# Optimization experiments

Hardware: AMD Instinct MI355X
Metric: run time of the kernel (lower is better)

The kernel has to match this reference:

```python
import jax, jax.numpy as jnp
import numpy as np

DIM = 512
HEADS = 8
HEAD_DIM = DIM // HEADS  # 64
NUM_ENC = 32             # num_encoding_channels
ENC_RANGE = 1.0
OFFSETS = (0, 512, 2560) # B=2 point clouds, num_points=(512, 2048)
B = len(OFFSETS) - 1
M = 2048                 # max num_points -> padded length
TOTAL = OFFSETS[-1]      # 2560 total points
ENC_IN = NUM_ENC * 3 + 3 # 99 (concat_input=True)


def setup_inputs() -> dict:
    key = jax.random.key(0)
    ks = jax.random.split(key, 6)
    return {
        "features": jax.random.normal(ks[0], (TOTAL, DIM), jnp.float32),
        "coordinates": jax.random.uniform(ks[1], (TOTAL, 3), jnp.float32),
        "qkv_w": jax.random.normal(ks[2], (3 * DIM, DIM), jnp.float32) * (DIM ** -0.5),
        "proj_w": jax.random.normal(ks[3], (DIM, DIM), jnp.float32) * (DIM ** -0.5),
        "proj_b": jnp.zeros((DIM,), jnp.float32),
        "pos_w": jax.random.normal(ks[4], (HEAD_DIM, ENC_IN), jnp.float32) * (ENC_IN ** -0.5),
        "pos_b": jnp.zeros((HEAD_DIM,), jnp.float32),
        "offsets": jnp.array(OFFSETS, jnp.int32),
    }


def reference(features, coordinates, qkv_w, proj_w, proj_b, pos_w, pos_b, offsets):
    # ragged -> padded index math (replaces cat_to_pad / pad_to_cat Python loops)
    pt = jnp.arange(TOTAL)
    b_idx = jnp.searchsorted(offsets, pt, side='right') - 1   # batch id per point
    w_idx = pt - offsets[b_idx]                                # within-batch position
    num_points = offsets[1:] - offsets[:-1]                    # [B]

    # SinusoidalEncoding(num_channels=32, concat_input=True) + Linear -> head_dim
    half = NUM_ENC // 2
    freqs = (2.0 ** jnp.arange(half, dtype=jnp.float32)) * jnp.pi / ENC_RANGE
    sc = coordinates[..., None] * freqs                        # [T, 3, half]
    enc = jnp.concatenate([jnp.sin(sc), jnp.cos(sc)], -1).reshape(TOTAL, 3 * NUM_ENC)
    enc = jnp.concatenate([enc, coordinates], -1)              # [T, 99]
    pos = enc @ pos_w.T + pos_b                                # [T, head_dim]

    feat_pad = jnp.zeros((B, M, DIM), features.dtype).at[b_idx, w_idx].set(features)
    pos_pad = jnp.zeros((B, M, HEAD_DIM), pos.dtype).at[b_idx, w_idx].set(pos)

    # offset_to_mask: mask[b, :, :offsets[b], :offsets[b]] = -inf (cumulative offsets!)
    r = jnp.arange(M)
    off_b = offsets[:-1]                                       # [B]
    blocked = (r[None, :, None] < off_b[:, None, None]) & (r[None, None, :] < off_b[:, None, None])
    mask = jnp.where(blocked, -jnp.inf, 0.0)[:, None]          # [B, 1, M, M]

    # attention
    qkv = (feat_pad @ qkv_w.T).reshape(B, M, 3, HEADS, HEAD_DIM)
    qkv = jnp.transpose(qkv, (2, 0, 3, 1, 4))                  # [3, B, H, M, hd]
    q, k, v = qkv[0], qkv[1], qkv[2]
    q = q + pos_pad[:, None]                                   # broadcast over heads
    k = k + pos_pad[:, None]
    scale = HEAD_DIM ** -0.5
    scores = jnp.einsum('bhqd,bhkd->bhqk', q, k) * scale + mask
    attn = jax.nn.softmax(scores, axis=-1)
    y = jnp.einsum('bhqk,bhkd->bhqd', attn, v)                 # [B, H, M, hd]
    y = jnp.transpose(y, (0, 2, 1, 3)).reshape(B, M, DIM)
    y = y @ proj_w.T + proj_b

    # zero_out_points: x[b, num_points[b]:] = 0
    valid = r[None, :] < num_points[:, None]
    y = jnp.where(valid[..., None], y, 0.0)

    # pad_to_cat back to ragged [total_N, C]
    return y[b_idx, w_idx]
```

## Files before the change

kernel.cpp:

```cpp
#include <hip/hip_runtime.h>
#include <math.h>

#define TOTAL 2560
#define NEG_BIG (-1e30f)
#define LOG2E_8 0.18033688011112042f

typedef __bf16 bf16x8 __attribute__((ext_vector_type(8)));
typedef float f32x4 __attribute__((ext_vector_type(4)));
typedef unsigned short ushort8v __attribute__((ext_vector_type(8)));
typedef unsigned short ushort4v __attribute__((ext_vector_type(4)));

__device__ inline unsigned short f2bf(float f) {
    unsigned u = __builtin_bit_cast(unsigned, f);
    u += 0x7fff + ((u >> 16) & 1);
    return (unsigned short)(u >> 16);
}

__device__ inline void gload16(const void* g, void* l) {
    __builtin_amdgcn_global_load_lds(
        (const __attribute__((address_space(1))) void*)g,
        (__attribute__((address_space(3))) void*)l, 16, 0, 0);
}

__global__ __launch_bounds__(256) void pos_cast_kernel(
    const float* __restrict__ coords,
    const float* __restrict__ pos_w,
    const float* __restrict__ pos_b,
    const float* __restrict__ f,  const float* __restrict__ qw, const float* __restrict__ pw,
    float* __restrict__ pos_out,
    unsigned short* __restrict__ fb, unsigned short* __restrict__ qwb, unsigned short* __restrict__ pwb)
{
    const int bx = blockIdx.x;
    if (bx < 640) {
        __shared__ float enc[4][100];
        const int wv   = threadIdx.x >> 6;
        const int lane = threadIdx.x & 63;
        const int p = bx * 4 + wv;
        const float c0 = coords[p * 3 + 0];
        const float c1 = coords[p * 3 + 1];
        const float c2 = coords[p * 3 + 2];
        for (int i = lane; i < 99; i += 64) {
            float v;
            if (i < 96) {
                const int d = i >> 5;
                const int j = i & 31;
                const float cv = (d == 0) ? c0 : ((d == 1) ? c1 : c2);
                const float freq = exp2f((float)(j & 15)) * 3.14159265358979323846f;
                const float sc = cv * freq;
                v = (j < 16) ? sinf(sc) : cosf(sc);
            } else {
                v = (i == 96) ? c0 : ((i == 97) ? c1 : c2);
            }
            enc[wv][i] = v;
        }
        float acc = pos_b[lane];
        const float* w = pos_w + lane * 99;
        for (int i = 0; i < 99; ++i) acc = fmaf(enc[wv][i], w[i], acc);
        pos_out[p * 64 + lane] = acc;
    } else {
        const int s = (bx - 640) * 256 + threadIdx.x;
        const float* src; unsigned short* dst; int ls;
        if (s < 163840)      { src = f;  dst = fb;  ls = s; }
        else if (s < 262144) { src = qw; dst = qwb; ls = s - 163840; }
        else                 { src = pw; dst = pwb; ls = s - 262144; }
        const float4 x0 = *(const float4*)(src + ls * 8);
        const float4 x1 = *(const float4*)(src + ls * 8 + 4);
        ushort8v o;
        o[0] = f2bf(x0.x); o[1] = f2bf(x0.y); o[2] = f2bf(x0.z); o[3] = f2bf(x0.w);
        o[4] = f2bf(x1.x); o[5] = f2bf(x1.y); o[6] = f2bf(x1.z); o[7] = f2bf(x1.w);
        *(ushort8v*)(dst + ls * 8) = o;
    }
}

__global__ __launch_bounds__(256) void qkv_mfma_kernel(
    const unsigned short* __restrict__ A,
    const unsigned short* __restrict__ Bm,
    const float* __restrict__ pos,
    unsigned short* __restrict__ q_ws,
    unsigned short* __restrict__ k_ws,
    unsigned short* __restrict__ vt_ws)
{
    __shared__ unsigned short Abuf[2][64 * 64];
    __shared__ unsigned short Bbuf[2][64 * 64];
    const int m0 = blockIdx.x * 64;
    const int n0 = blockIdx.y * 64;
    const int t = threadIdx.x;
    const int w = t >> 6, lane = t & 63;
    const int wr = w >> 1, wc = w & 1;
    const int c = lane & 15, g = lane >> 4;

    auto STAGE = [&](int kt, int cur) {
#pragma unroll
        for (int i = 0; i < 2; ++i) {
            const int off = w * 2048 + i * 1024;
            const int ba  = off + lane * 16;
            const int row = ba >> 7;
            const int slot = (ba & 127) >> 4;
            gload16(A  + (m0 + row) * 512 + kt * 64 + ((slot ^ (row & 7)) * 8),
                    (char*)&Abuf[cur][0] + off);
            gload16(Bm + (n0 + row) * 512 + kt * 64 + ((slot ^ (row & 7)) * 8),
                    (char*)&Bbuf[cur][0] + off);
        }
    };

    f32x4 acc[2][2];
#pragma unroll
    for (int mi = 0; mi < 2; ++mi)
#pragma unroll
        for (int ni = 0; ni < 2; ++ni) acc[mi][ni] = (f32x4){0.f, 0.f, 0.f, 0.f};

    STAGE(0, 0);
    int cur = 0;
    for (int kt = 0; kt < 8; ++kt) {
        __syncthreads();
        if (kt + 1 < 8) STAGE(kt + 1, cur ^ 1);
#pragma unroll
        for (int kk = 0; kk < 2; ++kk) {
            bf16x8 af[2], bfr[2];
#pragma unroll
            for (int mi = 0; mi < 2; ++mi) {
                const int row = wr * 32 + mi * 16 + c;
                af[mi] = *(const bf16x8*)&Abuf[cur][row * 64 + ((g + 4 * kk) ^ (row & 7)) * 8];
            }
#pragma unroll
            for (int ni = 0; ni < 2; ++ni) {
                const int row = wc * 32 + ni * 16 + c;
                bfr[ni] = *(const bf16x8*)&Bbuf[cur][row * 64 + ((g + 4 * kk) ^ (row & 7)) * 8];
            }
#pragma unroll
            for (int mi = 0; mi < 2; ++mi)
#pragma unroll
                for (int ni = 0; ni < 2; ++ni)
                    acc[mi][ni] = __builtin_amdgcn_mfma_f32_16x16x32_bf16(af[mi], bfr[ni], acc[mi][ni], 0, 0, 0);
        }
        cur ^= 1;
    }

    const int which = n0 >> 9;
    const int h = (n0 >> 6) & 7;
#pragma unroll
    for (int mi = 0; mi < 2; ++mi)
#pragma unroll
        for (int ni = 0; ni < 2; ++ni) {
            const int dd = wc * 32 + ni * 16 + c;
            const int p0 = m0 + wr * 32 + mi * 16 + 4 * g;
            if (which == 2) {
                ushort4v o4;
#pragma unroll
                for (int r = 0; r < 4; ++r) o4[r] = f2bf(acc[mi][ni][r]);
                *(ushort4v*)(vt_ws + (h * 64 + dd) * TOTAL + p0) = o4;
            } else {
#pragma unroll
                for (int r = 0; r < 4; ++r) {
                    const int p = p0 + r;
                    const float v = acc[mi][ni][r] + pos[p * 64 + dd];
                    const int idx = (h * TOTAL + p) * 64 + dd;
                    if (which == 0) q_ws[idx] = f2bf(v);
                    else            k_ws[idx] = f2bf(v);
                }
            }
        }
}

__global__ __launch_bounds__(256) void attn_kernel(
    const unsigned short* __restrict__ q_ws,
    const unsigned short* __restrict__ k_ws,
    const unsigned short* __restrict__ vt_ws,
    unsigned short* __restrict__ y)
{
    const int bx = blockIdx.x;
    const int h  = bx & 7;
    const int qt = bx >> 3;

    const int t    = threadIdx.x;
    const int w    = t >> 6;
    const int lane = t & 63;
    const int g    = lane >> 4;
    const int c    = lane & 15;
    const int c7   = c & 7;

    __shared__ unsigned short Kbuf[256 * 64];
    __shared__ unsigned short Vbuf[2][64 * 256];
    __shared__ unsigned short P_lds[64][264];

    const int nphase = (qt < 8) ? 2 : 1;
    int cur = 0;

    for (int phase = 0; phase < nphase; ++phase) {
        const int base = phase ? 0 : 512;
        const int nkt  = phase ? 2 : 8;
        const int kt0  = (!phase && qt < 8) ? 2 : 0;
        const float extra = phase ? 1536.0f : 0.0f;

        const unsigned short* Kg = k_ws + (h * TOTAL + base) * 64;
        const unsigned short* Vg = vt_ws + h * 64 * TOTAL + base;

        const unsigned short* Qrow = q_ws + ((h * TOTAL) + base + qt * 64 + 16 * w + c) * 64;
        const bf16x8 qa0 = *(const bf16x8*)(Qrow + 8 * g);
        const bf16x8 qa1 = *(const bf16x8*)(Qrow + 8 * g + 32);

        float m_old = NEG_BIG, l_old = 0.f;
        f32x4 o_acc[4];
#pragma unroll
        for (int n = 0; n < 4; ++n) o_acc[n] = (f32x4){0.f, 0.f, 0.f, 0.f};

        auto STAGE_K = [&](int kt) {
#pragma unroll
            for (int i = 0; i < 8; ++i) {
                const int off = w * 8192 + i * 1024;
                const int ba  = off + lane * 16;
                const int row = ba >> 7;
                const int slot = (ba & 127) >> 4;
                gload16(Kg + (kt * 256 + row) * 64 + ((slot ^ (row & 7)) * 8),
                        (char*)&Kbuf[0] + off);
            }
        };
        auto STAGE_V = [&](int kt, int vb) {
#pragma unroll
            for (int i = 0; i < 8; ++i) {
                const int off = w * 8192 + i * 1024;
                const int ba  = off + lane * 16;
                const int dd  = ba >> 9;
                const int slot = (ba & 511) >> 4;
                gload16(Vg + dd * TOTAL + kt * 256 + ((slot ^ (dd & 7)) * 8),
                        (char*)&Vbuf[vb][0] + off);
            }
        };

        if (phase) __syncthreads();
        STAGE_K(kt0);
        STAGE_V(kt0, cur);

        for (int kt = kt0; kt < nkt; ++kt) {
            __syncthreads();

            f32x4 s_acc[16];
#pragma unroll
            for (int n = 0; n < 16; ++n) {
                const int row = 16 * n + c;
                const bf16x8 kb0 = *(const bf16x8*)&Kbuf[row * 64 + ((g + 0) ^ c7) * 8];
                const bf16x8 kb1 = *(const bf16x8*)&Kbuf[row * 64 + ((g + 4) ^ c7) * 8];
                f32x4 a = __builtin_amdgcn_mfma_f32_16x16x32_bf16(kb0, qa0, (f32x4){0.f,0.f,0.f,0.f}, 0, 0, 0);
                s_acc[n] = __builtin_amdgcn_mfma_f32_16x16x32_bf16(kb1, qa1, a, 0, 0, 0);
            }
            __syncthreads();
            if (kt + 1 < nkt) STAGE_K(kt + 1);

            f32x4 m4 = s_acc[0];
#pragma unroll
            for (int n = 1; n < 16; ++n)
#pragma unroll
                for (int r = 0; r < 4; ++r) m4[r] = fmaxf(m4[r], s_acc[n][r]);
            float tm = fmaxf(fmaxf(m4[0], m4[1]), fmaxf(m4[2], m4[3])) * LOG2E_8;
            tm = fmaxf(tm, __shfl_xor(tm, 16));
            tm = fmaxf(tm, __shfl_xor(tm, 32));
            if (!__all(tm <= m_old + 8.0f)) {
                const float m_new = fmaxf(m_old, tm);
                const float corr = exp2f(m_old - m_new);
                float corr_r[4];
#pragma unroll
                for (int r = 0; r < 4; ++r) corr_r[r] = __shfl(corr, 4 * g + r);
#pragma unroll
                for (int n = 0; n < 4; ++n)
#pragma unroll
                    for (int r = 0; r < 4; ++r) o_acc[n][r] *= corr_r[r];
                l_old *= corr;
                m_old = m_new;
            }
            float rs = 0.f;
#pragma unroll
            for (int n = 0; n < 16; ++n)
#pragma unroll
                for (int r = 0; r < 4; ++r) {
                    const float pv = exp2f(fmaf(s_acc[n][r], LOG2E_8, -m_old));
                    s_acc[n][r] = pv;
                    rs += pv;
                }
            rs += __shfl_xor(rs, 16);
            rs += __shfl_xor(rs, 32);
            l_old += rs;

#pragma unroll
            for (int n = 0; n < 16; ++n) {
                ushort4v pk;
#pragma unroll
                for (int r = 0; r < 4; ++r) pk[r] = f2bf(s_acc[n][r]);
                *(ushort4v*)&P_lds[16 * w + c][16 * n + 4 * g] = pk;
            }

            if (kt + 1 < nkt) STAGE_V(kt + 1, cur ^ 1);

#pragma unroll
            for (int kk = 0; kk < 8; ++kk) {
                const bf16x8 pa = *(const bf16x8*)&P_lds[16 * w + c][8 * g + 32 * kk];
                const int vslot = (g + 4 * kk) ^ c7;
#pragma unroll
                for (int n = 0; n < 4; ++n) {
                    const bf16x8 vb = *(const bf16x8*)&Vbuf[cur][(16 * n + c) * 256 + vslot * 8];
                    o_acc[n] = __builtin_amdgcn_mfma_f32_16x16x32_bf16(pa, vb, o_acc[n], 0, 0, 0);
                }
            }
            cur ^= 1;
        }

        float inv_own;
        if (extra > 0.f) {
            const float mn  = fmaxf(m_old, 0.f);
            const float ccf = exp2f(m_old - mn);
            const float l   = l_old * ccf + extra * exp2f(-mn);
            inv_own = ccf / l;
        } else {
            inv_own = 1.0f / l_old;
        }
        float inv_r[4];
#pragma unroll
        for (int r = 0; r < 4; ++r) inv_r[r] = __shfl(inv_own, 4 * g + r);
        unsigned short* yb = y + (base + qt * 64 + 16 * w) * 512 + h * 64;
#pragma unroll
        for (int n = 0; n < 4; ++n)
#pragma unroll
            for (int r = 0; r < 4; ++r)
                yb[(4 * g + r) * 512 + 16 * n + c] = f2bf(o_acc[n][r] * inv_r[r]);
    }
}

__global__ __launch_bounds__(256) void proj_mfma_kernel(
    const unsigned short* __restrict__ A,
    const unsigned short* __restrict__ Bm,
    const float* __restrict__ bias,
    float* __restrict__ out)
{
    __shared__ unsigned short Abuf[2][64 * 64];
    __shared__ unsigned short Bbuf[2][64 * 64];
    const int m0 = blockIdx.x * 64;
    const int n0 = blockIdx.y * 64;
    const int t = threadIdx.x;
    const int w = t >> 6, lane = t & 63;
    const int wr = w >> 1, wc = w & 1;
    const int c = lane & 15, g = lane >> 4;

    auto STAGE = [&](int kt, int cur) {
#pragma unroll
        for (int i = 0; i < 2; ++i) {
            const int off = w * 2048 + i * 1024;
            const int ba  = off + lane * 16;
            const int row = ba >> 7;
            const int slot = (ba & 127) >> 4;
            gload16(A  + (m0 + row) * 512 + kt * 64 + ((slot ^ (row & 7)) * 8),
                    (char*)&Abuf[cur][0] + off);
            gload16(Bm + (n0 + row) * 512 + kt * 64 + ((slot ^ (row & 7)) * 8),
                    (char*)&Bbuf[cur][0] + off);
        }
    };

    f32x4 acc[2][2];
#pragma unroll
    for (int mi = 0; mi < 2; ++mi)
#pragma unroll
        for (int ni = 0; ni < 2; ++ni) acc[mi][ni] = (f32x4){0.f, 0.f, 0.f, 0.f};

    STAGE(0, 0);
    int cur = 0;
    for (int kt = 0; kt < 8; ++kt) {
        __syncthreads();
        if (kt + 1 < 8) STAGE(kt + 1, cur ^ 1);
#pragma unroll
        for (int kk = 0; kk < 2; ++kk) {
            bf16x8 af[2], bfr[2];
#pragma unroll
            for (int mi = 0; mi < 2; ++mi) {
                const int row = wr * 32 + mi * 16 + c;
                af[mi] = *(const bf16x8*)&Abuf[cur][row * 64 + ((g + 4 * kk) ^ (row & 7)) * 8];
            }
#pragma unroll
            for (int ni = 0; ni < 2; ++ni) {
                const int row = wc * 32 + ni * 16 + c;
                bfr[ni] = *(const bf16x8*)&Bbuf[cur][row * 64 + ((g + 4 * kk) ^ (row & 7)) * 8];
            }
#pragma unroll
            for (int mi = 0; mi < 2; ++mi)
#pragma unroll
                for (int ni = 0; ni < 2; ++ni)
                    acc[mi][ni] = __builtin_amdgcn_mfma_f32_16x16x32_bf16(af[mi], bfr[ni], acc[mi][ni], 0, 0, 0);
        }
        cur ^= 1;
    }

#pragma unroll
    for (int mi = 0; mi < 2; ++mi)
#pragma unroll
        for (int ni = 0; ni < 2; ++ni) {
            const int col = n0 + wc * 32 + ni * 16 + c;
            const float bv = bias[col];
#pragma unroll
            for (int r = 0; r < 4; ++r) {
                const int p = m0 + wr * 32 + mi * 16 + 4 * g + r;
                out[p * 512 + col] = acc[mi][ni][r] + bv;
            }
        }
}

extern "C" void kernel_launch(void* const* d_in, const int* in_sizes, int n_in,
                              void* d_out, int out_size, void* d_ws, size_t ws_size,
                              hipStream_t stream) {
    const float* features = (const float*)d_in[0];
    const float* coords   = (const float*)d_in[1];
    const float* qkv_w    = (const float*)d_in[2];
    const float* proj_w   = (const float*)d_in[3];
    const float* proj_b   = (const float*)d_in[4];
    const float* pos_w    = (const float*)d_in[5];
    const float* pos_b    = (const float*)d_in[6];
    float* out = (float*)d_out;

    float* pos_ws = (float*)d_ws;
    unsigned short* feat_bf  = (unsigned short*)(pos_ws + TOTAL * 64);
    unsigned short* qkvw_bf  = feat_bf + 2560 * 512;
    unsigned short* projw_bf = qkvw_bf + 1536 * 512;
    unsigned short* q_ws  = projw_bf + 512 * 512;
    unsigned short* k_ws  = q_ws  + 8 * TOTAL * 64;
    unsigned short* vt_ws = k_ws  + 8 * TOTAL * 64;
    unsigned short* y_bf  = vt_ws + 8 * TOTAL * 64;

    pos_cast_kernel<<<dim3(1792), dim3(256), 0, stream>>>(
        coords, pos_w, pos_b, features, qkv_w, proj_w,
        pos_ws, feat_bf, qkvw_bf, projw_bf);
    qkv_mfma_kernel<<<dim3(40, 24), dim3(256), 0, stream>>>(
        feat_bf, qkvw_bf, pos_ws, q_ws, k_ws, vt_ws);
    attn_kernel<<<dim3(256), dim3(256), 0, stream>>>(q_ws, k_ws, vt_ws, y_bf);
    proj_mfma_kernel<<<dim3(40, 8), dim3(256), 0, stream>>>(
        y_bf, projw_bf, proj_b, out);
}
```

Before: 64.41 us.

## Split attention over key range with partial softmax and combine kernel

The attention kernel now processes 128 query rows per block, two 16-row groups per wave, so each staged K/V tile is reused for twice as many queries. For the 2048-point cloud the key range is split into two halves across blocks, writing unnormalized fp32 partial outputs and (max, sum) statistics. A new combine kernel merges the halves and converts to bf16. The aim is better load balance and K/V reuse at the same grid size. The cost is an extra kernel launch and fp32 partial-output traffic through global memory.

```diff
diff --git a/kernel.cpp b/kernel.cpp
--- a/kernel.cpp
+++ b/kernel.cpp
@@ -162,15 +162,17 @@
         }
 }
 
-__global__ __launch_bounds__(256) void attn_kernel(
+__global__ __launch_bounds__(256) void attn_part_kernel(
     const unsigned short* __restrict__ q_ws,
     const unsigned short* __restrict__ k_ws,
     const unsigned short* __restrict__ vt_ws,
-    unsigned short* __restrict__ y)
+    float* __restrict__ o_part,
+    float2* __restrict__ ml2)
 {
-    const int bx = blockIdx.x;
-    const int h  = bx & 7;
-    const int qt = bx >> 3;
+    const int bx  = blockIdx.x;
+    const int h   = bx & 7;
+    const int qt2 = (bx >> 3) & 15;
+    const int sp  = bx >> 7;
 
     const int t    = threadIdx.x;
     const int w    = t >> 6;
@@ -183,26 +185,36 @@
     __shared__ unsigned short Vbuf[2][64 * 256];
     __shared__ unsigned short P_lds[64][264];
 
-    const int nphase = (qt < 8) ? 2 : 1;
+    const int nphase = (sp == 0 && qt2 < 4) ? 2 : 1;
     int cur = 0;
 
     for (int phase = 0; phase < nphase; ++phase) {
         const int base = phase ? 0 : 512;
-        const int nkt  = phase ? 2 : 8;
-        const int kt0  = (!phase && qt < 8) ? 2 : 0;
+        int t0, t1;
+        if (phase) { t0 = 0; t1 = 2; }
+        else {
+            const int kt0 = (qt2 < 4) ? 2 : 0;
+            t0 = sp ? 4 : kt0;
+            t1 = sp ? 8 : 4;
+        }
         const float extra = phase ? 1536.0f : 0.0f;
 
         const unsigned short* Kg = k_ws + (h * TOTAL + base) * 64;
         const unsigned short* Vg = vt_ws + h * 64 * TOTAL + base;
 
-        const unsigned short* Qrow = q_ws + ((h * TOTAL) + base + qt * 64 + 16 * w + c) * 64;
-        const bf16x8 qa0 = *(const bf16x8*)(Qrow + 8 * g);
-        const bf16x8 qa1 = *(const bf16x8*)(Qrow + 8 * g + 32);
-
-        float m_old = NEG_BIG, l_old = 0.f;
-        f32x4 o_acc[4];
-#pragma unroll
-        for (int n = 0; n < 4; ++n) o_acc[n] = (f32x4){0.f, 0.f, 0.f, 0.f};
+        const unsigned short* Qrow = q_ws + ((h * TOTAL) + base + qt2 * 128 + 32 * w + c) * 64;
+        const bf16x8 qlo0 = *(const bf16x8*)(Qrow + 8 * g);
+        const bf16x8 qlo1 = *(const bf16x8*)(Qrow + 8 * g + 32);
+        const bf16x8 qhi0 = *(const bf16x8*)(Qrow + 16 * 64 + 8 * g);
+        const bf16x8 qhi1 = *(const bf16x8*)(Qrow + 16 * 64 + 8 * g + 32);
+
+        float m_lo = NEG_BIG, l_lo = 0.f, m_hi = NEG_BIG, l_hi = 0.f;
+        f32x4 o_lo[4], o_hi[4];
+#pragma unroll
+        for (int n = 0; n < 4; ++n) {
+            o_lo[n] = (f32x4){0.f, 0.f, 0.f, 0.f};
+            o_hi[n] = (f32x4){0.f, 0.f, 0.f, 0.f};
+        }
 
         auto STAGE_K = [&](int kt) {
 #pragma unroll
@@ -227,30 +239,22 @@
             }
         };
 
-        if (phase) __syncthreads();
-        STAGE_K(kt0);
-        STAGE_V(kt0, cur);
-
-        for (int kt = kt0; kt < nkt; ++kt) {
-            __syncthreads();
-
-            f32x4 s_acc[16];
+        auto QK = [&](f32x4* s, const bf16x8& qa0, const bf16x8& qa1) {
 #pragma unroll
             for (int n = 0; n < 16; ++n) {
                 const int row = 16 * n + c;
                 const bf16x8 kb0 = *(const bf16x8*)&Kbuf[row * 64 + ((g + 0) ^ c7) * 8];
                 const bf16x8 kb1 = *(const bf16x8*)&Kbuf[row * 64 + ((g + 4) ^ c7) * 8];
                 f32x4 a = __builtin_amdgcn_mfma_f32_16x16x32_bf16(kb0, qa0, (f32x4){0.f,0.f,0.f,0.f}, 0, 0, 0);
-                s_acc[n] = __builtin_amdgcn_mfma_f32_16x16x32_bf16(kb1, qa1, a, 0, 0, 0);
-            }
-            __syncthreads();
-            if (kt + 1 < nkt) STAGE_K(kt + 1);
-
-            f32x4 m4 = s_acc[0];
+                s[n] = __builtin_amdgcn_mfma_f32_16x16x32_bf16(kb1, qa1, a, 0, 0, 0);
+            }
+        };
+        auto SOFTMAX = [&](f32x4* s, float& m_old, float& l_old, f32x4* o) {
+            f32x4 m4 = s[0];
 #pragma unroll
             for (int n = 1; n < 16; ++n)
 #pragma unroll
-                for (int r = 0; r < 4; ++r) m4[r] = fmaxf(m4[r], s_acc[n][r]);
+                for (int r = 0; r < 4; ++r) m4[r] = fmaxf(m4[r], s[n][r]);
             float tm = fmaxf(fmaxf(m4[0], m4[1]), fmaxf(m4[2], m4[3])) * LOG2E_8;
             tm = fmaxf(tm, __shfl_xor(tm, 16));
             tm = fmaxf(tm, __shfl_xor(tm, 32));
@@ -263,7 +267,7 @@
 #pragma unroll
                 for (int n = 0; n < 4; ++n)
 #pragma unroll
-                    for (int r = 0; r < 4; ++r) o_acc[n][r] *= corr_r[r];
+                    for (int r = 0; r < 4; ++r) o[n][r] *= corr_r[r];
                 l_old *= corr;
                 m_old = m_new;
             }
@@ -272,56 +276,132 @@
             for (int n = 0; n < 16; ++n)
 #pragma unroll
                 for (int r = 0; r < 4; ++r) {
-                    const float pv = exp2f(fmaf(s_acc[n][r], LOG2E_8, -m_old));
-                    s_acc[n][r] = pv;
+                    const float pv = exp2f(fmaf(s[n][r], LOG2E_8, -m_old));
+                    s[n][r] = pv;
                     rs += pv;
                 }
             rs += __shfl_xor(rs, 16);
             rs += __shfl_xor(rs, 32);
             l_old += rs;
-
+        };
+        auto PWRITE = [&](const f32x4* s) {
 #pragma unroll
             for (int n = 0; n < 16; ++n) {
                 ushort4v pk;
 #pragma unroll
-                for (int r = 0; r < 4; ++r) pk[r] = f2bf(s_acc[n][r]);
+                for (int r = 0; r < 4; ++r) pk[r] = f2bf(s[n][r]);
                 *(ushort4v*)&P_lds[16 * w + c][16 * n + 4 * g] = pk;
             }
-
-            if (kt + 1 < nkt) STAGE_V(kt + 1, cur ^ 1);
-
+        };
+        auto PV = [&](f32x4* o, int vb) {
 #pragma unroll
             for (int kk = 0; kk < 8; ++kk) {
                 const bf16x8 pa = *(const bf16x8*)&P_lds[16 * w + c][8 * g + 32 * kk];
                 const int vslot = (g + 4 * kk) ^ c7;
 #pragma unroll
                 for (int n = 0; n < 4; ++n) {
-                    const bf16x8 vb = *(const bf16x8*)&Vbuf[cur][(16 * n + c) * 256 + vslot * 8];
-                    o_acc[n] = __builtin_amdgcn_mfma_f32_16x16x32_bf16(pa, vb, o_acc[n], 0, 0, 0);
+                    const bf16x8 vv = *(const bf16x8*)&Vbuf[vb][(16 * n + c) * 256 + vslot * 8];
+                    o[n] = __builtin_amdgcn_mfma_f32_16x16x32_bf16(pa, vv, o[n], 0, 0, 0);
                 }
             }
+        };
+
+        if (phase) __syncthreads();
+        STAGE_K(t0);
+        STAGE_V(t0, cur);
+
+        for (int kt = t0; kt < t1; ++kt) {
+            __syncthreads();
+            f32x4 s_acc[16];
+            QK(s_acc, qlo0, qlo1);
+            SOFTMAX(s_acc, m_lo, l_lo, o_lo);
+            PWRITE(s_acc);
+            QK(s_acc, qhi0, qhi1);
+            __syncthreads();
+            if (kt + 1 < t1) STAGE_K(kt + 1);
+            PV(o_lo, cur);
+            SOFTMAX(s_acc, m_hi, l_hi, o_hi);
+            PWRITE(s_acc);
+            if (kt + 1 < t1) STAGE_V(kt + 1, cur ^ 1);
+            PV(o_hi, cur);
             cur ^= 1;
         }
 
-        float inv_own;
-        if (extra > 0.f) {
-            const float mn  = fmaxf(m_old, 0.f);
-            const float ccf = exp2f(m_old - mn);
-            const float l   = l_old * ccf + extra * exp2f(-mn);
-            inv_own = ccf / l;
+        if (phase) {
+            const float mn_l = fmaxf(m_lo, 0.f);
+            const float cl   = exp2f(m_lo - mn_l);
+            const float il   = cl / (l_lo * cl + extra * exp2f(-mn_l));
+            const float mn_h = fmaxf(m_hi, 0.f);
+            const float ch   = exp2f(m_hi - mn_h);
+            const float ih   = ch / (l_hi * ch + extra * exp2f(-mn_h));
+            float ilr[4], ihr[4];
+#pragma unroll
+            for (int r = 0; r < 4; ++r) {
+                ilr[r] = __shfl(il, 4 * g + r);
+                ihr[r] = __shfl(ih, 4 * g + r);
+            }
+            float* op = o_part + (size_t)(qt2 * 128 + 32 * w) * 512 + h * 64;
+#pragma unroll
+            for (int n = 0; n < 4; ++n)
+#pragma unroll
+                for (int r = 0; r < 4; ++r) {
+                    op[(4 * g + r) * 512 + 16 * n + c]      = o_lo[n][r] * ilr[r];
+                    op[(16 + 4 * g + r) * 512 + 16 * n + c] = o_hi[n][r] * ihr[r];
+                }
         } else {
-            inv_own = 1.0f / l_old;
-        }
-        float inv_r[4];
-#pragma unroll
-        for (int r = 0; r < 4; ++r) inv_r[r] = __shfl(inv_own, 4 * g + r);
-        unsigned short* yb = y + (base + qt * 64 + 16 * w) * 512 + h * 64;
-#pragma unroll
-        for (int n = 0; n < 4; ++n)
-#pragma unroll
-            for (int r = 0; r < 4; ++r)
-                yb[(4 * g + r) * 512 + 16 * n + c] = f2bf(o_acc[n][r] * inv_r[r]);
+            float* op = o_part + (size_t)sp * (TOTAL * 512)
+                      + (size_t)(512 + qt2 * 128 + 32 * w) * 512 + h * 64;
+#pragma unroll
+            for (int n = 0; n < 4; ++n)
+#pragma unroll
+                for (int r = 0; r < 4; ++r) {
+                    op[(4 * g + r) * 512 + 16 * n + c]      = o_lo[n][r];
+                    op[(16 + 4 * g + r) * 512 + 16 * n + c] = o_hi[n][r];
+                }
+            if (lane < 16) {
+                const int p = 512 + qt2 * 128 + 32 * w + c;
+                ml2[((size_t)sp * TOTAL + p) * 8 + h]      = make_float2(m_lo, l_lo);
+                ml2[((size_t)sp * TOTAL + p + 16) * 8 + h] = make_float2(m_hi, l_hi);
+            }
+        }
     }
+}
+
+__global__ __launch_bounds__(256) void combine_kernel(
+    const float* __restrict__ o_part,
+    const float2* __restrict__ ml2,
+    unsigned short* __restrict__ y)
+{
+    const int e = blockIdx.x * 256 + threadIdx.x;
+    const int p = e >> 6;
+    const int seg = e & 63;
+    const size_t bo = (size_t)p * 512 + seg * 8;
+    const float4 a0 = *(const float4*)(o_part + bo);
+    const float4 a1 = *(const float4*)(o_part + bo + 4);
+    ushort8v y8;
+    if (p < 512) {
+        y8[0] = f2bf(a0.x); y8[1] = f2bf(a0.y); y8[2] = f2bf(a0.z); y8[3] = f2bf(a0.w);
+        y8[4] = f2bf(a1.x); y8[5] = f2bf(a1.y); y8[6] = f2bf(a1.z); y8[7] = f2bf(a1.w);
+    } else {
+        const int h = seg >> 3;
+        const float2 v0 = ml2[(size_t)p * 8 + h];
+        const float2 v1 = ml2[(size_t)(TOTAL + p) * 8 + h];
+        const float mt = fmaxf(v0.x, v1.x);
+        const float c0 = exp2f(v0.x - mt), c1 = exp2f(v1.x - mt);
+        const float inv = 1.0f / fmaf(v0.y, c0, v1.y * c1);
+        const float f0 = c0 * inv, f1 = c1 * inv;
+        const float4 b0 = *(const float4*)(o_part + (size_t)TOTAL * 512 + bo);
+        const float4 b1 = *(const float4*)(o_part + (size_t)TOTAL * 512 + bo + 4);
+        y8[0] = f2bf(fmaf(a0.x, f0, b0.x * f1));
+        y8[1] = f2bf(fmaf(a0.y, f0, b0.y * f1));
+        y8[2] = f2bf(fmaf(a0.z, f0, b0.z * f1));
+        y8[3] = f2bf(fmaf(a0.w, f0, b0.w * f1));
+        y8[4] = f2bf(fmaf(a1.x, f0, b1.x * f1));
+        y8[5] = f2bf(fmaf(a1.y, f0, b1.y * f1));
+        y8[6] = f2bf(fmaf(a1.z, f0, b1.z * f1));
+        y8[7] = f2bf(fmaf(a1.w, f0, b1.w * f1));
+    }
+    *(ushort8v*)(y + bo) = y8;
 }
 
 __global__ __launch_bounds__(256) void proj_mfma_kernel(
@@ -419,14 +499,18 @@
     unsigned short* q_ws  = projw_bf + 512 * 512;
     unsigned short* k_ws  = q_ws  + 8 * TOTAL * 64;
     unsigned short* vt_ws = k_ws  + 8 * TOTAL * 64;
-    unsigned short* y_bf  = vt_ws + 8 * TOTAL * 64;
+    float* o_part = (float*)(vt_ws + 8 * TOTAL * 64);
+    float2* ml2   = (float2*)(o_part + 2 * TOTAL * 512);
+    unsigned short* y_bf = (unsigned short*)(ml2 + 2 * TOTAL * 8);
 
     pos_cast_kernel<<<dim3(1792), dim3(256), 0, stream>>>(
         coords, pos_w, pos_b, features, qkv_w, proj_w,
         pos_ws, feat_bf, qkvw_bf, projw_bf);
     qkv_mfma_kernel<<<dim3(40, 24), dim3(256), 0, stream>>>(
         feat_bf, qkvw_bf, pos_ws, q_ws, k_ws, vt_ws);
-    attn_kernel<<<dim3(256), dim3(256), 0, stream>>>(q_ws, k_ws, vt_ws, y_bf);
+    attn_part_kernel<<<dim3(256), dim3(256), 0, stream>>>(
+        q_ws, k_ws, vt_ws, o_part, ml2);
+    combine_kernel<<<dim3(640), dim3(256), 0, stream>>>(o_part, ml2, y_bf);
     proj_mfma_kernel<<<dim3(40, 8), dim3(256), 0, stream>>>(
         y_bf, projw_bf, proj_b, out);
 }
```

Measured after the change: 78.59 us. +22.0%, slower.

## Split attention key tile across two wave groups with LDS softmax merge

Applied to the files above, without the earlier changes.

Doubles the attention block to 512 threads. Each group of four waves processes half of every 256-key tile, and the two partial online-softmax states (max, sum, output) are merged through shared memory at the end. This aims to raise wave-level parallelism and latency hiding per CU, since the grid has only 256 blocks. In exchange it adds shared memory (Om, Oml), a merge pass and a barrier. Each wave tracks its own running max, so the rescaling logic is duplicated.

```diff
diff --git a/kernel.cpp b/kernel.cpp
--- a/kernel.cpp
+++ b/kernel.cpp
@@ -162,7 +162,7 @@
         }
 }
 
-__global__ __launch_bounds__(256) void attn_kernel(
+__global__ __launch_bounds__(512) void attn_kernel(
     const unsigned short* __restrict__ q_ws,
     const unsigned short* __restrict__ k_ws,
     const unsigned short* __restrict__ vt_ws,
@@ -174,6 +174,9 @@
 
     const int t    = threadIdx.x;
     const int w    = t >> 6;
+    const int wp   = w & 3;
+    const int half = w >> 2;
+    const int koff = half * 128;
     const int lane = t & 63;
     const int g    = lane >> 4;
     const int c    = lane & 15;
@@ -182,6 +185,8 @@
     __shared__ unsigned short Kbuf[256 * 64];
     __shared__ unsigned short Vbuf[2][64 * 256];
     __shared__ unsigned short P_lds[64][264];
+    __shared__ float  Om[64 * 64];
+    __shared__ float2 Oml[64];
 
     const int nphase = (qt < 8) ? 2 : 1;
     int cur = 0;
@@ -195,7 +200,7 @@
         const unsigned short* Kg = k_ws + (h * TOTAL + base) * 64;
         const unsigned short* Vg = vt_ws + h * 64 * TOTAL + base;
 
-        const unsigned short* Qrow = q_ws + ((h * TOTAL) + base + qt * 64 + 16 * w + c) * 64;
+        const unsigned short* Qrow = q_ws + ((h * TOTAL) + base + qt * 64 + 16 * wp + c) * 64;
         const bf16x8 qa0 = *(const bf16x8*)(Qrow + 8 * g);
         const bf16x8 qa1 = *(const bf16x8*)(Qrow + 8 * g + 32);
 
@@ -206,8 +211,8 @@
 
         auto STAGE_K = [&](int kt) {
 #pragma unroll
-            for (int i = 0; i < 8; ++i) {
-                const int off = w * 8192 + i * 1024;
+            for (int i = 0; i < 4; ++i) {
+                const int off = w * 4096 + i * 1024;
                 const int ba  = off + lane * 16;
                 const int row = ba >> 7;
                 const int slot = (ba & 127) >> 4;
@@ -217,8 +222,8 @@
         };
         auto STAGE_V = [&](int kt, int vb) {
 #pragma unroll
-            for (int i = 0; i < 8; ++i) {
-                const int off = w * 8192 + i * 1024;
+            for (int i = 0; i < 4; ++i) {
+                const int off = w * 4096 + i * 1024;
                 const int ba  = off + lane * 16;
                 const int dd  = ba >> 9;
                 const int slot = (ba & 511) >> 4;
@@ -234,10 +239,10 @@
         for (int kt = kt0; kt < nkt; ++kt) {
             __syncthreads();
 
-            f32x4 s_acc[16];
-#pragma unroll
-            for (int n = 0; n < 16; ++n) {
-                const int row = 16 * n + c;
+            f32x4 s_acc[8];
+#pragma unroll
+            for (int n = 0; n < 8; ++n) {
+                const int row = koff + 16 * n + c;
                 const bf16x8 kb0 = *(const bf16x8*)&Kbuf[row * 64 + ((g + 0) ^ c7) * 8];
                 const bf16x8 kb1 = *(const bf16x8*)&Kbuf[row * 64 + ((g + 4) ^ c7) * 8];
                 f32x4 a = __builtin_amdgcn_mfma_f32_16x16x32_bf16(kb0, qa0, (f32x4){0.f,0.f,0.f,0.f}, 0, 0, 0);
@@ -248,7 +253,7 @@
 
             f32x4 m4 = s_acc[0];
 #pragma unroll
-            for (int n = 1; n < 16; ++n)
+            for (int n = 1; n < 8; ++n)
 #pragma unroll
                 for (int r = 0; r < 4; ++r) m4[r] = fmaxf(m4[r], s_acc[n][r]);
             float tm = fmaxf(fmaxf(m4[0], m4[1]), fmaxf(m4[2], m4[3])) * LOG2E_8;
@@ -269,7 +274,7 @@
             }
             float rs = 0.f;
 #pragma unroll
-            for (int n = 0; n < 16; ++n)
+            for (int n = 0; n < 8; ++n)
 #pragma unroll
                 for (int r = 0; r < 4; ++r) {
                     const float pv = exp2f(fmaf(s_acc[n][r], LOG2E_8, -m_old));
@@ -281,46 +286,69 @@
             l_old += rs;
 
 #pragma unroll
-            for (int n = 0; n < 16; ++n) {
+            for (int n = 0; n < 8; ++n) {
                 ushort4v pk;
 #pragma unroll
                 for (int r = 0; r < 4; ++r) pk[r] = f2bf(s_acc[n][r]);
-                *(ushort4v*)&P_lds[16 * w + c][16 * n + 4 * g] = pk;
+                *(ushort4v*)&P_lds[16 * wp + c][koff + 16 * n + 4 * g] = pk;
             }
 
             if (kt + 1 < nkt) STAGE_V(kt + 1, cur ^ 1);
 
 #pragma unroll
-            for (int kk = 0; kk < 8; ++kk) {
-                const bf16x8 pa = *(const bf16x8*)&P_lds[16 * w + c][8 * g + 32 * kk];
-                const int vslot = (g + 4 * kk) ^ c7;
+            for (int kk = 0; kk < 4; ++kk) {
+                const bf16x8 pa = *(const bf16x8*)&P_lds[16 * wp + c][koff + 8 * g + 32 * kk];
+                const int vgrp = ((koff >> 3) + 4 * kk + g) ^ c7;
 #pragma unroll
                 for (int n = 0; n < 4; ++n) {
-                    const bf16x8 vb = *(const bf16x8*)&Vbuf[cur][(16 * n + c) * 256 + vslot * 8];
+                    const bf16x8 vb = *(const bf16x8*)&Vbuf[cur][(16 * n + c) * 256 + vgrp * 8];
                     o_acc[n] = __builtin_amdgcn_mfma_f32_16x16x32_bf16(pa, vb, o_acc[n], 0, 0, 0);
                 }
             }
             cur ^= 1;
         }
 
-        float inv_own;
-        if (extra > 0.f) {
-            const float mn  = fmaxf(m_old, 0.f);
-            const float ccf = exp2f(m_old - mn);
-            const float l   = l_old * ccf + extra * exp2f(-mn);
-            inv_own = ccf / l;
-        } else {
-            inv_own = 1.0f / l_old;
-        }
-        float inv_r[4];
-#pragma unroll
-        for (int r = 0; r < 4; ++r) inv_r[r] = __shfl(inv_own, 4 * g + r);
-        unsigned short* yb = y + (base + qt * 64 + 16 * w) * 512 + h * 64;
-#pragma unroll
-        for (int n = 0; n < 4; ++n)
-#pragma unroll
-            for (int r = 0; r < 4; ++r)
-                yb[(4 * g + r) * 512 + 16 * n + c] = f2bf(o_acc[n][r] * inv_r[r]);
+        if (half == 1) {
+            const int pr = wp * 16;
+#pragma unroll
+            for (int n = 0; n < 4; ++n)
+#pragma unroll
+                for (int r = 0; r < 4; ++r)
+                    Om[(pr + 4 * g + r) * 64 + 16 * n + c] = o_acc[n][r];
+            if (g == 0) Oml[pr + c] = make_float2(m_old, l_old);
+        }
+        __syncthreads();
+        if (half == 0) {
+            const int pr = wp * 16;
+            const float2 o2 = Oml[pr + c];
+            const float mm = fmaxf(m_old, o2.x);
+            const float f0 = exp2f(m_old - mm), f1 = exp2f(o2.x - mm);
+            float l = l_old * f0 + o2.y * f1;
+            float so = 1.f;
+            if (extra > 0.f) {
+                const float mn = fmaxf(mm, 0.f);
+                const float cc = exp2f(mm - mn);
+                l = l * cc + extra * exp2f(-mn);
+                so = cc;
+            }
+            const float inv = so / l;
+            const float a0 = f0 * inv, a1 = f1 * inv;
+            float a0r[4], a1r[4];
+#pragma unroll
+            for (int r = 0; r < 4; ++r) {
+                a0r[r] = __shfl(a0, 4 * g + r);
+                a1r[r] = __shfl(a1, 4 * g + r);
+            }
+            unsigned short* yb = y + (base + qt * 64 + 16 * wp) * 512 + h * 64;
+#pragma unroll
+            for (int n = 0; n < 4; ++n)
+#pragma unroll
+                for (int r = 0; r < 4; ++r) {
+                    const float o1v = Om[(pr + 4 * g + r) * 64 + 16 * n + c];
+                    yb[(4 * g + r) * 512 + 16 * n + c] =
+                        f2bf(o_acc[n][r] * a0r[r] + o1v * a1r[r]);
+                }
+        }
     }
 }
 
@@ -426,7 +454,7 @@
         pos_ws, feat_bf, qkvw_bf, projw_bf);
     qkv_mfma_kernel<<<dim3(40, 24), dim3(256), 0, stream>>>(
         feat_bf, qkvw_bf, pos_ws, q_ws, k_ws, vt_ws);
-    attn_kernel<<<dim3(256), dim3(256), 0, stream>>>(q_ws, k_ws, vt_ws, y_bf);
+    attn_kernel<<<dim3(256), dim3(512), 0, stream>>>(q_ws, k_ws, vt_ws, y_bf);
     proj_mfma_kernel<<<dim3(40, 8), dim3(256), 0, stream>>>(
         y_bf, projw_bf, proj_b, out);
 }
```

Measured after the change: 58.03 us. 1.11x faster.
